# Kernel optimization log

Measured on AMD Instinct MI355X. Metric: run time of the kernel, lower is better.

Reference implementation:

```python
import jax, jax.numpy as jnp
import numpy as np

B, T, S, H, V, MAXL = 8, 128, 256, 1024, 32000, 512
STD = 0.02


def _ln(x, g, b):
    m = jnp.mean(x, -1, keepdims=True)
    v = jnp.mean((x - m) ** 2, -1, keepdims=True)
    return (x - m) / jnp.sqrt(v + 1e-5) * g + b


def setup_inputs() -> dict:
    key = jax.random.key(0)
    ks = jax.random.split(key, 16)
    n = lambda k, shape: jax.random.normal(k, shape, jnp.float32) * STD
    inp = {
        "input_ids": jax.random.randint(ks[0], (B, T), 0, V),
        "encoder_hidden_states": jax.random.normal(ks[1], (B, S, H), jnp.float32),
        "pattern_masks": jax.random.randint(ks[2], (B, T, V), 0, 2).astype(bool),
        "attention_mask": jnp.ones((B, S), bool),
        "tok_emb": n(ks[3], (V, H)),
        "pos_emb": n(ks[4], (MAXL, H)),
        "w_ih": n(ks[5], (4 * H, H)),
        "w_hh": n(ks[6], (4 * H, H)),
        "b_ih": jnp.zeros((4 * H,), jnp.float32),
        "b_hh": jnp.zeros((4 * H,), jnp.float32),
        "wq": n(ks[7], (H, H)), "bq": jnp.zeros((H,), jnp.float32),
        "wk": n(ks[8], (H, H)), "bk": jnp.zeros((H,), jnp.float32),
        "wc": n(ks[9], (H, 2 * H)), "bc": jnp.zeros((H,), jnp.float32),
        "wo": n(ks[10], (V, H)), "bo": jnp.zeros((V,), jnp.float32),
        "g1": n(ks[11], (H,)), "be1": jnp.zeros((H,), jnp.float32),
        "g2": n(ks[12], (H,)), "be2": jnp.zeros((H,), jnp.float32),
    }
    return inp


def reference(input_ids, encoder_hidden_states, pattern_masks, attention_mask,
              tok_emb, pos_emb, w_ih, w_hh, b_ih, b_hh,
              wq, bq, wk, bk, wc, bc, wo, bo, g1, be1, g2, be2):
    # Token + positional embedding (dropout is identity in eval)
    x = tok_emb[input_ids] + pos_emb[:T][None, :, :]  # [B,T,H]

    # Single-layer LSTM (PyTorch gate order i,f,g,o) via scan over time
    def step(carry, xt):
        h, c = carry
        gates = xt @ w_ih.T + b_ih + h @ w_hh.T + b_hh
        i, f, g, o = jnp.split(gates, 4, axis=-1)
        c = jax.nn.sigmoid(f) * c + jax.nn.sigmoid(i) * jnp.tanh(g)
        h = jax.nn.sigmoid(o) * jnp.tanh(c)
        return (h, c), h

    h0 = jnp.zeros((B, H), x.dtype)
    _, hs = jax.lax.scan(step, (h0, h0), jnp.swapaxes(x, 0, 1))
    lstm_out = jnp.swapaxes(hs, 0, 1)  # [B,T,H]

    # Attention: per-position loop in torch == batched over T (keys invariant)
    qn = _ln(lstm_out @ wq.T + bq, g1, be1)              # [B,T,H]
    kn = _ln(encoder_hidden_states @ wk.T + bk, g1, be1)  # [B,S,H]
    scale = H ** (-0.5) * 0.5
    scores = jnp.einsum('bth,bsh->bts', qn, kn) * scale
    am = attention_mask[:, None, :]
    scores = jnp.where(am, scores, -10000.0)
    mx = jnp.max(scores, -1, keepdims=True)
    ex = jnp.exp(scores - mx)
    ex = jnp.where(am, ex, 0.0)
    w = ex / (jnp.sum(ex, -1, keepdims=True) + 1e-6)
    ctx = jnp.einsum('bts,bsh->bth', w, kn)              # [B,T,H]

    hidden = _ln(jnp.concatenate([lstm_out, ctx], -1) @ wc.T + bc, g2, be2)
    logits = hidden @ wo.T + bo                           # [B,T,V]
    logits = jnp.where(pattern_masks, logits, -10000.0)
    return logits
```

## Files before the change

kernel.cpp:

```cpp
#include <hip/hip_runtime.h>
#include <cstdint>
#include <cstddef>

#define Bdim 8
#define Tdim 128
#define Sdim 256
#define Hdim 1024
#define Vdim 32000
#define SENT 0xFFFFFFFFFFFFFFFFULL

typedef unsigned short u16;
typedef unsigned long long u64;
typedef __attribute__((ext_vector_type(8))) short short8;
typedef __attribute__((ext_vector_type(4))) short short4v;
typedef __attribute__((ext_vector_type(4))) float f32x4;
typedef __attribute__((ext_vector_type(2))) unsigned long long u64x2;

union Frag { short8 v; short4v h[2]; };

__device__ __forceinline__ float bf2f(u16 u){
  union { unsigned int i; float f; } x; x.i = ((unsigned int)u) << 16; return x.f;
}
__device__ __forceinline__ u16 f2b(float f){
  union { float f; unsigned int u; } x; x.f = f;
  unsigned int r = x.u + 0x7FFFu + ((x.u >> 16) & 1u);
  return (u16)(r >> 16);
}
__device__ __forceinline__ float ftanh(float x){
  x = fminf(10.f, fmaxf(-10.f, x));
  const float e = __expf(2.f * x);
  return (e - 1.f) / (e + 1.f);
}

__device__ __forceinline__ void gload16(const void* g, void* l){
  __builtin_amdgcn_global_load_lds((const __attribute__((address_space(1))) unsigned int*)g,
                                   (__attribute__((address_space(3))) unsigned int*)l, 16, 0, 0);
}

__device__ __forceinline__ int qsw(int r){ return (r + (r >> 2)) & 3; }

__device__ __forceinline__ u64 aload(const u64* p){
  return __hip_atomic_load(p, __ATOMIC_RELAXED, __HIP_MEMORY_SCOPE_AGENT);
}
__device__ __forceinline__ void astore(u64* p, u64 v){
  __hip_atomic_store(p, v, __ATOMIC_RELAXED, __HIP_MEMORY_SCOPE_AGENT);
}

__global__ __launch_bounds__(256) void detect_bool_k(const unsigned char* __restrict__ p, int* __restrict__ flag){
  __shared__ int s;
  if (threadIdx.x == 0) s = 0;
  __syncthreads();
  int loc = 0;
  for (int i = threadIdx.x; i < 65536; i += 256)
    if ((i & 3) && p[i]) loc = 1;
  if (loc) atomicOr(&s, 1);
  __syncthreads();
  if (threadIdx.x == 0) flag[0] = s;
}

__device__ __forceinline__ bool mask_at(const void* m, size_t idx, int byteflag){
  if (byteflag) return ((const unsigned char*)m)[idx] != 0;
  return ((const int*)m)[idx] != 0;
}

template<typename OutT, bool BF32, int MASK, int NT>
__device__ __forceinline__ void gemm_core(
    char* ldsA0, char* ldsB0, char* ldsA1, char* ldsB1,
    int m0, int n0, int z,
    const u16* __restrict__ A, int lda, long sA,
    const void* __restrict__ Bp, int ldb, long sB,
    OutT* __restrict__ C, int ldc, long sC,
    const float* __restrict__ bias,
    const void* __restrict__ mask,
    const int* __restrict__ mflag,
    int K, float alpha)
{
  const int tid  = threadIdx.x;
  const int lane = tid & 63, wid = tid >> 6;
  const int lm = lane & 15, lg = lane >> 4;
  const int wm = wid >> 1, wn = wid & 1;
  const char* Ab = (const char*)(A + (size_t)z * sA);

  f32x4 acc[4][4 * NT];
#pragma unroll
  for (int i = 0; i < 4; i++)
#pragma unroll
    for (int j = 0; j < 4 * NT; j++) acc[i][j] = (f32x4){0.f, 0.f, 0.f, 0.f};

  const int brow = tid >> 1, bhalf = tid & 1;
  const int qb_st = qsw(brow);

  auto stageA = [&](char* dst, int k0){
    const char* ga = Ab + ((size_t)m0 * lda + k0) * 2;
    const int f0 = tid, f1 = tid + 256;
    const int r0 = f0 >> 2, r1 = f1 >> 2;
    gload16(ga + (size_t)r0 * (lda * 2) + ((f0 & 3) ^ qsw(r0)) * 16, dst + (f0 & ~63) * 16);
    gload16(ga + (size_t)r1 * (lda * 2) + ((f1 & 3) ^ qsw(r1)) * 16, dst + (f1 & ~63) * 16);
  };
  auto stageB16 = [&](char* dst, int k0){
    const char* gbase = (const char*)((const u16*)Bp + (size_t)z * sB);
#pragma unroll
    for (int s = 0; s < NT; s++) {
      const char* gb = gbase + ((size_t)(n0 + s * 128) * ldb + k0) * 2;
      const int f0 = tid, f1 = tid + 256;
      const int r0 = f0 >> 2, r1 = f1 >> 2;
      gload16(gb + (size_t)r0 * (ldb * 2) + ((f0 & 3) ^ qsw(r0)) * 16, dst + s * 8192 + (f0 & ~63) * 16);
      gload16(gb + (size_t)r1 * (ldb * 2) + ((f1 & 3) ^ qsw(r1)) * 16, dst + s * 8192 + (f1 & ~63) * 16);
    }
  };

  float4 nv0, nv1, nv2, nv3;
  auto loadB32 = [&](int k0){
    const float* Bf = (const float*)Bp + (size_t)z * sB;
    const float4* src = (const float4*)(Bf + (size_t)(n0 + brow) * ldb + k0 + bhalf * 16);
    nv0 = src[0]; nv1 = src[1]; nv2 = src[2]; nv3 = src[3];
  };
  auto writeB32 = [&](char* dst){
    union { short8 v; short s[8]; } p0, p1;
    p0.s[0]=(short)f2b(nv0.x); p0.s[1]=(short)f2b(nv0.y); p0.s[2]=(short)f2b(nv0.z); p0.s[3]=(short)f2b(nv0.w);
    p0.s[4]=(short)f2b(nv1.x); p0.s[5]=(short)f2b(nv1.y); p0.s[6]=(short)f2b(nv1.z); p0.s[7]=(short)f2b(nv1.w);
    p1.s[0]=(short)f2b(nv2.x); p1.s[1]=(short)f2b(nv2.y); p1.s[2]=(short)f2b(nv2.z); p1.s[3]=(short)f2b(nv2.w);
    p1.s[4]=(short)f2b(nv3.x); p1.s[5]=(short)f2b(nv3.y); p1.s[6]=(short)f2b(nv3.z); p1.s[7]=(short)f2b(nv3.w);
    char* base = dst + brow * 64;
    *(short8*)(base + (((bhalf * 2 + 0) ^ qb_st) * 16)) = p0.v;
    *(short8*)(base + (((bhalf * 2 + 1) ^ qb_st) * 16)) = p1.v;
  };

  stageA(ldsA0, 0);
  if (BF32) { loadB32(0); writeB32(ldsB0); }
  else stageB16(ldsB0, 0);
  __syncthreads();

  char *cA = ldsA0, *cB = ldsB0, *nA = ldsA1, *nB = ldsB1;
  const int nk = K >> 5;
  for (int i = 0; i < nk; i++) {
    const bool more = (i + 1) < nk;
    if (more) {
      stageA(nA, (i + 1) << 5);
      if (BF32) loadB32((i + 1) << 5);
      else stageB16(nB, (i + 1) << 5);
    }
    Frag a[4];
#pragma unroll
    for (int mi = 0; mi < 4; mi++) {
      const int rr = wm * 64 + mi * 16 + lm;
      const int q = qsw(rr);
      const char* p = cA + rr * 64 + (lg & 1) * 8;
      a[mi].h[0] = *(const short4v*)(p + (((lg >> 1) ^ q) * 16));
      a[mi].h[1] = *(const short4v*)(p + ((((lg >> 1) | 2) ^ q) * 16));
    }
#pragma unroll
    for (int ni = 0; ni < 4 * NT; ni++) {
      const int s = ni >> 2, nl = ni & 3;
      const int rr = wn * 64 + nl * 16 + lm;
      const int q = qsw(rr);
      const char* p = cB + s * 8192 + rr * 64 + (lg & 1) * 8;
      Frag b;
      b.h[0] = *(const short4v*)(p + (((lg >> 1) ^ q) * 16));
      b.h[1] = *(const short4v*)(p + ((((lg >> 1) | 2) ^ q) * 16));
#pragma unroll
      for (int mi = 0; mi < 4; mi++)
        acc[mi][ni] = __builtin_amdgcn_mfma_f32_16x16x32_bf16(a[mi].v, b.v, acc[mi][ni], 0, 0, 0);
    }
    if (BF32 && more) writeB32(nB);
    __syncthreads();
    char* t;
    t = cA; cA = nA; nA = t;
    t = cB; cB = nB; nB = t;
  }

  const int bflag = (MASK == 1) ? *mflag : 0;
#pragma unroll
  for (int mi = 0; mi < 4; mi++) {
#pragma unroll
    for (int ni = 0; ni < 4 * NT; ni++) {
      const int row = m0 + wm * 64 + mi * 16 + lg * 4;
      const int col = n0 + (ni >> 2) * 128 + wn * 64 + (ni & 3) * 16 + lm;
      const float bb = bias ? bias[col] : 0.f;
#pragma unroll
      for (int j = 0; j < 4; j++) {
        float v = acc[mi][ni][j] * alpha + bb;
        const size_t midx = (size_t)(row + j) * ldc + col;
        if (MASK == 1) { if (!mask_at(mask, midx, bflag)) v = -10000.0f; }
        if (MASK == 2) { if (!((const unsigned char*)mask)[midx]) v = -10000.0f; }
        const size_t o = (size_t)z * sC + midx;
        if constexpr (sizeof(OutT) == 2) C[o] = (OutT)f2b(v); else C[o] = (OutT)v;
      }
    }
  }
}

template<typename OutT, bool BF32, int MASK, bool SWAP, int NT = 1>
__global__ __launch_bounds__(256) void gemm_bt(
    const u16* __restrict__ A, int lda, long sA,
    const void* __restrict__ Bp, int ldb, long sB,
    OutT* __restrict__ C, int ldc, long sC,
    const float* __restrict__ bias,
    const void* __restrict__ mask,
    const int* __restrict__ mflag,
    int K, float alpha)
{
  __shared__ alignas(16) char lds[(8192 + 8192 * NT) * 2];
  const int m0 = (SWAP ? blockIdx.x : blockIdx.y) * 128;
  const int n0 = (SWAP ? blockIdx.y : blockIdx.x) * (128 * NT);
  char* ldsA1 = lds + 8192 + 8192 * NT;
  gemm_core<OutT, BF32, MASK, NT>(lds, lds + 8192, ldsA1, ldsA1 + 8192,
      m0, n0, blockIdx.z, A, lda, sA, Bp, ldb, sB, C, ldc, sC,
      bias, mask, mflag, K, alpha);
}

__device__ void lstm_body(char* smem,
    const u16* __restrict__ xpre, const u16* __restrict__ whh,
    u16* __restrict__ hbuf, int bx)
{
  u16* wlds = (u16*)smem;
  u16* hlds = (u16*)(smem + 131072);
  const int tid = threadIdx.x, lane = tid & 63, wid = tid >> 6;
  const int lm = lane & 15, lg = lane >> 4;
  const int gcol0 = bx * 64;

  for (int q = tid; q < 8192; q += 256) {
    const int r = q >> 7, cc = q & 127;
    gload16(whh + (size_t)(gcol0 + r) * 1024 + (size_t)(cc ^ (r & 7)) * 8,
            (char*)wlds + (q & ~63) * 16);
  }

  float c_reg = 0.f;
  const int rloc = wid * 16 + lm, swb = rloc & 7, swa = lm & 7;
  const u16* wl = wlds + rloc * 1024;
  const u16* hl = hlds + swa * 1024;
  const int pk = tid >> 2, qq = tid & 3;
  const u16* xp = xpre + (size_t)(lm * Tdim) * 4096 + gcol0 + wid * 16 + lg * 4;

  for (int t = 0; t < Tdim; t++) {
    u64 xw = 0;
    if (lm < 8) xw = *(const u64*)(xp + (size_t)t * 4096);
    if (t > 0) {
      const u64* ps = (const u64*)(hbuf + ((size_t)(t - 1) * 64 + pk) * 128) + qq * 8;
      u64 w0=SENT,w1=SENT,w2=SENT,w3=SENT,w4=SENT,w5=SENT,w6=SENT,w7=SENT;
      for (;;) {
        if (w0 == SENT) w0 = aload(ps + 0);
        if (w1 == SENT) w1 = aload(ps + 1);
        if (w2 == SENT) w2 = aload(ps + 2);
        if (w3 == SENT) w3 = aload(ps + 3);
        if (w4 == SENT) w4 = aload(ps + 4);
        if (w5 == SENT) w5 = aload(ps + 5);
        if (w6 == SENT) w6 = aload(ps + 6);
        if (w7 == SENT) w7 = aload(ps + 7);
        if (w0 != SENT && w1 != SENT && w2 != SENT && w3 != SENT &&
            w4 != SENT && w5 != SENT && w6 != SENT && w7 != SENT) break;
        __builtin_amdgcn_s_sleep(1);
      }
      {
        const int m = qq * 2;
        u64x2 a; a[0] = w0; a[1] = w1;
        u64x2 b; b[0] = w2; b[1] = w3;
        *(u64x2*)((char*)hlds + m * 2048 + (((pk * 2 + 0) ^ m) * 16)) = a;
        *(u64x2*)((char*)hlds + m * 2048 + (((pk * 2 + 1) ^ m) * 16)) = b;
      }
      {
        const int m = qq * 2 + 1;
        u64x2 a; a[0] = w4; a[1] = w5;
        u64x2 b; b[0] = w6; b[1] = w7;
        *(u64x2*)((char*)hlds + m * 2048 + (((pk * 2 + 0) ^ m) * 16)) = a;
        *(u64x2*)((char*)hlds + m * 2048 + (((pk * 2 + 1) ^ m) * 16)) = b;
      }
    }
    __syncthreads();

    f32x4 acc0, acc1, acc2, acc3;
    {
      union { u64 w; u16 s[4]; } xu; xu.w = xw;
      acc0[0] = bf2f(xu.s[0]); acc0[1] = bf2f(xu.s[1]);
      acc0[2] = bf2f(xu.s[2]); acc0[3] = bf2f(xu.s[3]);
    }
    acc1 = (f32x4){0.f,0.f,0.f,0.f};
    acc2 = (f32x4){0.f,0.f,0.f,0.f};
    acc3 = (f32x4){0.f,0.f,0.f,0.f};

    if (t > 0) {
#pragma unroll
      for (int kk = 0; kk < 32; kk++) {
        const int c0 = kk * 4 + (lg >> 1);
        const int sub = (lg & 1) * 4;
        Frag aw, bh;
        aw.h[0] = *(const short4v*)(wl + ((c0 ^ swb) << 3) + sub);
        aw.h[1] = *(const short4v*)(wl + (((c0 + 2) ^ swb) << 3) + sub);
        bh.h[0] = *(const short4v*)(hl + ((c0 ^ swa) << 3) + sub);
        bh.h[1] = *(const short4v*)(hl + (((c0 + 2) ^ swa) << 3) + sub);
        if ((kk & 3) == 0)      acc0 = __builtin_amdgcn_mfma_f32_16x16x32_bf16(aw.v, bh.v, acc0, 0, 0, 0);
        else if ((kk & 3) == 1) acc1 = __builtin_amdgcn_mfma_f32_16x16x32_bf16(aw.v, bh.v, acc1, 0, 0, 0);
        else if ((kk & 3) == 2) acc2 = __builtin_amdgcn_mfma_f32_16x16x32_bf16(aw.v, bh.v, acc2, 0, 0, 0);
        else                    acc3 = __builtin_amdgcn_mfma_f32_16x16x32_bf16(aw.v, bh.v, acc3, 0, 0, 0);
      }
    }
    const f32x4 g4 = (acc0 + acc1) + (acc2 + acc3);

    const float si = 1.f / (1.f + __expf(-g4[0]));
    const float sf = 1.f / (1.f + __expf(-g4[1]));
    const float so = 1.f / (1.f + __expf(-g4[3]));
    const float cn = sf * c_reg + si * ftanh(g4[2]);
    c_reg = cn;
    const float hn = so * ftanh(cn);
    const int hb = (int)f2b(hn);

    const int v0 = __shfl(hb, lm, 64);
    const int v1 = __shfl(hb, lm + 16, 64);
    const int v2 = __shfl(hb, lm + 32, 64);
    const int v3 = __shfl(hb, lm + 48, 64);
    if (lg == 0 && lm < 8) {
      const u64 pack = (u64)(v0 & 0xFFFF) | ((u64)(v1 & 0xFFFF) << 16)
                     | ((u64)(v2 & 0xFFFF) << 32) | ((u64)(v3 & 0xFFFF) << 48);
      astore((u64*)(hbuf + ((size_t)t * 64 + bx) * 128 + lm * 16 + wid * 4), pack);
    }
    __syncthreads();
  }
}

__global__ __launch_bounds__(256) void lstm_plus(
    const u16* __restrict__ xpre, const u16* __restrict__ whh,
    u16* __restrict__ hbuf,
    const u16* __restrict__ encb, const u16* __restrict__ wkb,
    float* __restrict__ klin, const float* __restrict__ bk,
    const float* __restrict__ wo, u16* __restrict__ wob,
    const void* __restrict__ pmask, unsigned char* __restrict__ pmaskb,
    const int* __restrict__ bflag)
{
  __shared__ alignas(16) char smem[147456];
  const int bx = blockIdx.x;
  if (bx < 64) {
    lstm_body(smem, xpre, whh, hbuf, bx);
  } else if (bx < 192) {
    const int idx = bx - 64;
    gemm_core<float, false, 0, 1>(smem, smem + 8192, smem + 16384, smem + 24576,
        (idx >> 3) * 128, (idx & 7) * 128, 0,
        encb, 1024, 0, wkb, 1024, 0, klin, 1024, 0, bk, nullptr, nullptr, 1024, 1.f);
  } else {
    const int s = bx - 192;
    const int tid = threadIdx.x;
    if (wob) {
      for (int r = s; r < Vdim; r += 64) {
        const size_t i = (size_t)r * 1024 + tid * 4;
        const float4 v = *(const float4*)(wo + i);
        u16* op = wob + i;
        op[0] = f2b(v.x); op[1] = f2b(v.y); op[2] = f2b(v.z); op[3] = f2b(v.w);
      }
    }
    if (pmaskb) {
      const int bfl = *bflag;
      const size_t total = (size_t)Bdim * Tdim * Vdim;
      const size_t nthr = 64 * 256;
      if (bfl == 0) {
        for (size_t i = ((size_t)s * 256 + tid) * 4; i < total; i += nthr * 4) {
          const int4 v = *(const int4*)((const int*)pmask + i);
          uchar4 o;
          o.x = v.x ? 1 : 0; o.y = v.y ? 1 : 0; o.z = v.z ? 1 : 0; o.w = v.w ? 1 : 0;
          *(uchar4*)(pmaskb + i) = o;
        }
      } else {
        for (size_t i = ((size_t)s * 256 + tid) * 16; i < total; i += nthr * 16) {
          *(int4*)(pmaskb + i) = *(const int4*)((const unsigned char*)pmask + i);
        }
      }
    }
  }
}

__global__ __launch_bounds__(256) void hbuf_cat_k(const u16* __restrict__ hbuf, u16* __restrict__ cat){
  const int t = blockIdx.x, tid = threadIdx.x;
  const int p = tid >> 2, q = tid & 3;
  const u64* src = (const u64*)(hbuf + ((size_t)t * 64 + p) * 128);
#pragma unroll
  for (int m = 0; m < 8; m++) {
    const u64 v = src[m * 4 + q];
    *(u64*)(cat + (size_t)(m * Tdim + t) * 2048 + p * 16 + q * 4) = v;
  }
}

__global__ __launch_bounds__(256) void prep_k(
    const float* __restrict__ w_hh, const float* __restrict__ w_ih,
    const float* __restrict__ wq,   const float* __restrict__ wk,
    const float* __restrict__ wc,   const float* __restrict__ enc,
    const int* __restrict__ ids,
    const float* __restrict__ tok,  const float* __restrict__ pos,
    const float* __restrict__ b_ih, const float* __restrict__ b_hh,
    u16* __restrict__ whhb, u16* __restrict__ wihb,
    u16* __restrict__ wqb,  u16* __restrict__ wkb,  u16* __restrict__ wcb,
    u16* __restrict__ encb, u16* __restrict__ xbf,
    float* __restrict__ biasf, u64* __restrict__ hbuf)
{
  const int b = blockIdx.x, tid = threadIdx.x;
  if (b < 8192) {
    const bool ih = b >= 4096;
    const int r = b & 4095;
    const int p = (r & 3) * Hdim + (r >> 2);
    const float4 v = *(const float4*)((ih ? w_ih : w_hh) + (size_t)p * Hdim + tid * 4);
    u16* op = (ih ? wihb : whhb) + (size_t)r * Hdim + tid * 4;
    op[0] = f2b(v.x); op[1] = f2b(v.y); op[2] = f2b(v.z); op[3] = f2b(v.w);
  } else if (b < 9216) {
    const size_t i = (size_t)(b - 8192) * 1024 + tid * 4;
    const float4 v = *(const float4*)(wq + i);
    u16* op = wqb + i;
    op[0] = f2b(v.x); op[1] = f2b(v.y); op[2] = f2b(v.z); op[3] = f2b(v.w);
  } else if (b < 10240) {
    const size_t i = (size_t)(b - 9216) * 1024 + tid * 4;
    const float4 v = *(const float4*)(wk + i);
    u16* op = wkb + i;
    op[0] = f2b(v.x); op[1] = f2b(v.y); op[2] = f2b(v.z); op[3] = f2b(v.w);
  } else if (b < 12288) {
    const size_t i = (size_t)(b - 10240) * 1024 + tid * 4;
    const float4 v = *(const float4*)(wc + i);
    u16* op = wcb + i;
    op[0] = f2b(v.x); op[1] = f2b(v.y); op[2] = f2b(v.z); op[3] = f2b(v.w);
  } else if (b < 14336) {
    const size_t i = (size_t)(b - 12288) * 1024 + tid * 4;
    const float4 v = *(const float4*)(enc + i);
    u16* op = encb + i;
    op[0] = f2b(v.x); op[1] = f2b(v.y); op[2] = f2b(v.z); op[3] = f2b(v.w);
  } else if (b < 15360) {
    const int row = b - 14336;
    const int t = row & (Tdim - 1);
    const int id = ids[row];
    const int h0 = tid * 4;
    const float4 a = *(const float4*)(tok + (size_t)id * Hdim + h0);
    const float4 p = *(const float4*)(pos + (size_t)t * Hdim + h0);
    u16* op = xbf + (size_t)row * Hdim + h0;
    op[0] = f2b(a.x + p.x); op[1] = f2b(a.y + p.y); op[2] = f2b(a.z + p.z); op[3] = f2b(a.w + p.w);
  } else if (b < 15364) {
    const int n0 = (b - 15360) * 1024 + tid * 4;
#pragma unroll
    for (int j = 0; j < 4; j++) {
      const int n = n0 + j;
      const int p = (n & 3) * Hdim + (n >> 2);
      biasf[n] = b_ih[p] + b_hh[p];
    }
  } else {
    const size_t i = ((size_t)(b - 15364) * 256 + tid) * 4;
    u64x2 s2; s2[0] = SENT; s2[1] = SENT;
    *(u64x2*)(hbuf + i)     = s2;
    *(u64x2*)(hbuf + i + 2) = s2;
  }
}

__global__ __launch_bounds__(256) void ln_rows(const float* __restrict__ in, u16* __restrict__ out,
                                               const float* __restrict__ g, const float* __restrict__ be){
  const int row = blockIdx.x, tid = threadIdx.x;
  const int lane = tid & 63, wid = tid >> 6;
  const float4 x = *(const float4*)(in + (size_t)row * Hdim + tid * 4);
  float s = x.x + x.y + x.z + x.w;
  float q = x.x * x.x + x.y * x.y + x.z * x.z + x.w * x.w;
  for (int o = 32; o; o >>= 1) { s += __shfl_down(s, o, 64); q += __shfl_down(q, o, 64); }
  __shared__ float sm[8];
  if (lane == 0) { sm[wid] = s; sm[4 + wid] = q; }
  __syncthreads();
  const float ts = sm[0] + sm[1] + sm[2] + sm[3];
  const float tq = sm[4] + sm[5] + sm[6] + sm[7];
  const float mean = ts * (1.f / Hdim);
  const float var  = tq * (1.f / Hdim) - mean * mean;
  const float r = rsqrtf(var + 1e-5f);
  const int h0 = tid * 4;
  const float4 gv = *(const float4*)(g + h0);
  const float4 bv = *(const float4*)(be + h0);
  u16* op = out + (size_t)row * Hdim + h0;
  op[0] = f2b((x.x - mean) * r * gv.x + bv.x);
  op[1] = f2b((x.y - mean) * r * gv.y + bv.y);
  op[2] = f2b((x.z - mean) * r * gv.z + bv.z);
  op[3] = f2b((x.w - mean) * r * gv.w + bv.w);
}
__global__ __launch_bounds__(256) void softmax_k(const float* __restrict__ sc, const void* __restrict__ am,
                                                 const int* __restrict__ mflag, u16* __restrict__ w){
  const int row = blockIdx.x, tid = threadIdx.x;
  const int lane = tid & 63, wid = tid >> 6;
  const int b = row >> 7;
  const int bflag = *mflag;
  const float v = sc[(size_t)row * Sdim + tid];
  const bool mk = mask_at(am, (size_t)b * Sdim + tid, bflag);
  const float vm = mk ? v : -10000.0f;
  float mx = vm;
  for (int o = 32; o; o >>= 1) mx = fmaxf(mx, __shfl_down(mx, o, 64));
  __shared__ float sm[8];
  if (lane == 0) sm[wid] = mx;
  __syncthreads();
  mx = fmaxf(fmaxf(sm[0], sm[1]), fmaxf(sm[2], sm[3]));
  const float ex = mk ? expf(vm - mx) : 0.f;
  float ss = ex;
  for (int o = 32; o; o >>= 1) ss += __shfl_down(ss, o, 64);
  if (lane == 0) sm[4 + wid] = ss;
  __syncthreads();
  const float tot = sm[4] + sm[5] + sm[6] + sm[7];
  w[(size_t)row * Sdim + tid] = f2b(ex / (tot + 1e-6f));
}
__global__ __launch_bounds__(256) void transp_k(const u16* __restrict__ kn, u16* __restrict__ knT){
  __shared__ u16 tile[64][65];
  const int b = blockIdx.z, h0 = blockIdx.x * 64, s0 = blockIdx.y * 64;
  const u16* src = kn  + (size_t)b * Sdim * Hdim;
  u16* dst       = knT + (size_t)b * Hdim * Sdim;
  for (int e = threadIdx.x; e < 4096; e += 256) {
    const int r = e >> 6, c = e & 63;
    tile[r][c] = src[(size_t)(s0 + r) * Hdim + h0 + c];
  }
  __syncthreads();
  for (int e = threadIdx.x; e < 4096; e += 256) {
    const int hr = e >> 6, scc = e & 63;
    dst[(size_t)(h0 + hr) * Sdim + s0 + scc] = tile[scc][hr];
  }
}

extern "C" void kernel_launch(void* const* d_in, const int* in_sizes, int n_in,
                              void* d_out, int out_size, void* d_ws, size_t ws_size,
                              hipStream_t stream) {
  const int*   input_ids = (const int*)d_in[0];
  const float* enc   = (const float*)d_in[1];
  const void*  pmask = d_in[2];
  const void*  amask = d_in[3];
  const float* tok  = (const float*)d_in[4];
  const float* pos  = (const float*)d_in[5];
  const float* w_ih = (const float*)d_in[6];
  const float* w_hh = (const float*)d_in[7];
  const float* b_ih = (const float*)d_in[8];
  const float* b_hh = (const float*)d_in[9];
  const float* wq = (const float*)d_in[10];
  const float* bq = (const float*)d_in[11];
  const float* wk = (const float*)d_in[12];
  const float* bk = (const float*)d_in[13];
  const float* wc = (const float*)d_in[14];
  const float* bc = (const float*)d_in[15];
  const float* wo = (const float*)d_in[16];
  const float* bo = (const float*)d_in[17];
  const float* g1  = (const float*)d_in[18];
  const float* be1 = (const float*)d_in[19];
  const float* g2  = (const float*)d_in[20];
  const float* be2 = (const float*)d_in[21];
  float* out = (float*)d_out;

  char* ws = (char*)d_ws;
  size_t off = 0;
  auto alloc = [&](size_t b){ size_t o = off; off += (b + 255) & ~(size_t)255; return o; };
  u16*   whhb  = (u16*)  (ws + alloc((size_t)4096 * 1024 * 2));
  u16*   wihb  = (u16*)  (ws + alloc((size_t)4096 * 1024 * 2));
  u16*   wqb   = (u16*)  (ws + alloc((size_t)1024 * 1024 * 2));
  u16*   wkb   = (u16*)  (ws + alloc((size_t)1024 * 1024 * 2));
  u16*   wcb   = (u16*)  (ws + alloc((size_t)1024 * 2048 * 2));
  float* biasf = (float*)(ws + alloc(4096 * 4));
  u16*   xbf   = (u16*)  (ws + alloc((size_t)1024 * 1024 * 2));
  u16*   encb  = (u16*)  (ws + alloc((size_t)2048 * 1024 * 2));
  u16*   xpre  = (u16*)  (ws + alloc((size_t)1024 * 4096 * 2));
  u16*   hbuf  = (u16*)  (ws + alloc((size_t)Tdim * 64 * 128 * 2));
  u16*   cat   = (u16*)  (ws + alloc((size_t)1024 * 2048 * 2));
  float* qlin  = (float*)(ws + alloc((size_t)1024 * 1024 * 4));
  u16*   qn    = (u16*)  (ws + alloc((size_t)1024 * 1024 * 2));
  float* klin  = (float*)(ws + alloc((size_t)2048 * 1024 * 4));
  u16*   kn    = (u16*)  (ws + alloc((size_t)2048 * 1024 * 2));
  u16*   knT   = (u16*)  (ws + alloc((size_t)2048 * 1024 * 2));
  float* scores= (float*)(ws + alloc((size_t)8 * 128 * 256 * 4));
  u16*   attw  = (u16*)  (ws + alloc((size_t)8 * 128 * 256 * 2));
  float* hlin  = (float*)(ws + alloc((size_t)1024 * 1024 * 4));
  u16*   hid   = (u16*)  (ws + alloc((size_t)1024 * 1024 * 2));
  int*   bflag = (int*)  (ws + alloc(256));
  unsigned char* pmaskb = (unsigned char*)(ws + alloc((size_t)Bdim * Tdim * Vdim));
  const bool havePak = off <= ws_size;
  u16*   wob   = (u16*)  (ws + alloc((size_t)Vdim * Hdim * 2));
  const bool haveWob = off <= ws_size;
  if (!havePak) pmaskb = nullptr;
  if (!haveWob) wob = nullptr;
  (void)in_sizes; (void)n_in; (void)out_size;

  detect_bool_k<<<1, 256, 0, stream>>>((const unsigned char*)pmask, bflag);
  prep_k<<<15620, 256, 0, stream>>>(w_hh, w_ih, wq, wk, wc, enc, input_ids,
      tok, pos, b_ih, b_hh, whhb, wihb, wqb, wkb, wcb, encb, xbf, biasf, (u64*)hbuf);

  gemm_bt<u16, false, 0, false><<<dim3(32, 8, 1), 256, 0, stream>>>(
      xbf, 1024, 0, wihb, 1024, 0, xpre, 4096, 0, biasf, nullptr, nullptr, 1024, 1.f);

  lstm_plus<<<256, 256, 0, stream>>>(xpre, whhb, hbuf, encb, wkb, klin, bk,
                                     wo, wob, pmask, pmaskb, bflag);
  hbuf_cat_k<<<Tdim, 256, 0, stream>>>(hbuf, cat);

  gemm_bt<float, false, 0, false><<<dim3(8, 8, 1), 256, 0, stream>>>(
      cat, 2048, 0, wqb, 1024, 0, qlin, 1024, 0, bq, nullptr, nullptr, 1024, 1.f);
  ln_rows<<<1024, 256, 0, stream>>>(qlin, qn, g1, be1);
  ln_rows<<<2048, 256, 0, stream>>>(klin, kn, g1, be1);
  transp_k<<<dim3(16, 4, 8), 256, 0, stream>>>(kn, knT);

  gemm_bt<float, false, 0, false><<<dim3(2, 1, 8), 256, 0, stream>>>(
      qn, 1024, 131072, kn, 1024, 262144, scores, 256, 32768, nullptr, nullptr, nullptr, 1024, 0.015625f);
  softmax_k<<<1024, 256, 0, stream>>>(scores, amask, bflag, attw);
  gemm_bt<u16, false, 0, false><<<dim3(8, 1, 8), 256, 0, stream>>>(
      attw, 256, 32768, knT, 256, 262144, cat + 1024, 2048, 262144, nullptr, nullptr, nullptr, 256, 1.f);

  gemm_bt<float, false, 0, false><<<dim3(8, 8, 1), 256, 0, stream>>>(
      cat, 2048, 0, wcb, 2048, 0, hlin, 1024, 0, bc, nullptr, nullptr, 2048, 1.f);
  ln_rows<<<1024, 256, 0, stream>>>(hlin, hid, g2, be2);

  if (wob && pmaskb)
    gemm_bt<float, false, 2, true, 2><<<dim3(8, 125, 1), 256, 0, stream>>>(
        hid, 1024, 0, wob, 1024, 0, out, 32000, 0, bo, pmaskb, nullptr, 1024, 1.f);
  else if (wob)
    gemm_bt<float, false, 1, true, 2><<<dim3(8, 125, 1), 256, 0, stream>>>(
        hid, 1024, 0, wob, 1024, 0, out, 32000, 0, bo, pmask, bflag, 1024, 1.f);
  else
    gemm_bt<float, true, 1, true><<<dim3(8, 250, 1), 256, 0, stream>>>(
        hid, 1024, 0, wo, 1024, 0, out, 32000, 0, bo, pmask, bflag, 1024, 1.f);
}
```

Before: 842.9 us.

## Fold small kernels into prep and LSTM launches, shrink output GEMM tile

The bool-detection kernel becomes an extra block of prep_k, and the hbuf-to-cat copy kernel is removed because the LSTM blocks now write their hidden states straight into the concat buffer. The wq and wc bf16 conversions move out of prep_k into the idle side blocks of the LSTM launch, where they overlap the recurrent loop. The final vocab GEMM goes from an NT=2 tile to NT=1, doubling its grid. This cuts launch count and serial prep work, at the cost of extra stores inside the latency-bound LSTM loop and less B-tile reuse in the large GEMM.

```diff
diff --git a/kernel.cpp b/kernel.cpp
--- a/kernel.cpp
+++ b/kernel.cpp
@@ -44,18 +44,6 @@
 }
 __device__ __forceinline__ void astore(u64* p, u64 v){
   __hip_atomic_store(p, v, __ATOMIC_RELAXED, __HIP_MEMORY_SCOPE_AGENT);
-}
-
-__global__ __launch_bounds__(256) void detect_bool_k(const unsigned char* __restrict__ p, int* __restrict__ flag){
-  __shared__ int s;
-  if (threadIdx.x == 0) s = 0;
-  __syncthreads();
-  int loc = 0;
-  for (int i = threadIdx.x; i < 65536; i += 256)
-    if ((i & 3) && p[i]) loc = 1;
-  if (loc) atomicOr(&s, 1);
-  __syncthreads();
-  if (threadIdx.x == 0) flag[0] = s;
 }
 
 __device__ __forceinline__ bool mask_at(const void* m, size_t idx, int byteflag){
@@ -211,7 +199,7 @@
 
 __device__ void lstm_body(char* smem,
     const u16* __restrict__ xpre, const u16* __restrict__ whh,
-    u16* __restrict__ hbuf, int bx)
+    u16* __restrict__ hbuf, u16* __restrict__ cat, int bx)
 {
   u16* wlds = (u16*)smem;
   u16* hlds = (u16*)(smem + 131072);
@@ -312,6 +300,7 @@
       const u64 pack = (u64)(v0 & 0xFFFF) | ((u64)(v1 & 0xFFFF) << 16)
                      | ((u64)(v2 & 0xFFFF) << 32) | ((u64)(v3 & 0xFFFF) << 48);
       astore((u64*)(hbuf + ((size_t)t * 64 + bx) * 128 + lm * 16 + wid * 4), pack);
+      *(u64*)(cat + (size_t)(lm * Tdim + t) * 2048 + bx * 16 + wid * 4) = pack;
     }
     __syncthreads();
   }
@@ -319,17 +308,19 @@
 
 __global__ __launch_bounds__(256) void lstm_plus(
     const u16* __restrict__ xpre, const u16* __restrict__ whh,
-    u16* __restrict__ hbuf,
+    u16* __restrict__ hbuf, u16* __restrict__ cat,
     const u16* __restrict__ encb, const u16* __restrict__ wkb,
     float* __restrict__ klin, const float* __restrict__ bk,
     const float* __restrict__ wo, u16* __restrict__ wob,
+    const float* __restrict__ wq, u16* __restrict__ wqb,
+    const float* __restrict__ wc, u16* __restrict__ wcb,
     const void* __restrict__ pmask, unsigned char* __restrict__ pmaskb,
     const int* __restrict__ bflag)
 {
   __shared__ alignas(16) char smem[147456];
   const int bx = blockIdx.x;
   if (bx < 64) {
-    lstm_body(smem, xpre, whh, hbuf, bx);
+    lstm_body(smem, xpre, whh, hbuf, cat, bx);
   } else if (bx < 192) {
     const int idx = bx - 64;
     gemm_core<float, false, 0, 1>(smem, smem + 8192, smem + 16384, smem + 24576,
@@ -338,6 +329,21 @@
   } else {
     const int s = bx - 192;
     const int tid = threadIdx.x;
+    for (int r = s; r < 1024; r += 64) {
+      const size_t i = (size_t)r * 1024 + tid * 4;
+      const float4 v = *(const float4*)(wq + i);
+      u16* op = wqb + i;
+      op[0] = f2b(v.x); op[1] = f2b(v.y); op[2] = f2b(v.z); op[3] = f2b(v.w);
+    }
+    for (int r = s; r < 1024; r += 64) {
+#pragma unroll
+      for (int hc = 0; hc < 2; hc++) {
+        const size_t i = (size_t)r * 2048 + hc * 1024 + tid * 4;
+        const float4 v = *(const float4*)(wc + i);
+        u16* op = wcb + i;
+        op[0] = f2b(v.x); op[1] = f2b(v.y); op[2] = f2b(v.z); op[3] = f2b(v.w);
+      }
+    }
     if (wob) {
       for (int r = s; r < Vdim; r += 64) {
         const size_t i = (size_t)r * 1024 + tid * 4;
@@ -366,29 +372,18 @@
   }
 }
 
-__global__ __launch_bounds__(256) void hbuf_cat_k(const u16* __restrict__ hbuf, u16* __restrict__ cat){
-  const int t = blockIdx.x, tid = threadIdx.x;
-  const int p = tid >> 2, q = tid & 3;
-  const u64* src = (const u64*)(hbuf + ((size_t)t * 64 + p) * 128);
-#pragma unroll
-  for (int m = 0; m < 8; m++) {
-    const u64 v = src[m * 4 + q];
-    *(u64*)(cat + (size_t)(m * Tdim + t) * 2048 + p * 16 + q * 4) = v;
-  }
-}
-
 __global__ __launch_bounds__(256) void prep_k(
     const float* __restrict__ w_hh, const float* __restrict__ w_ih,
-    const float* __restrict__ wq,   const float* __restrict__ wk,
-    const float* __restrict__ wc,   const float* __restrict__ enc,
+    const float* __restrict__ wk,   const float* __restrict__ enc,
     const int* __restrict__ ids,
     const float* __restrict__ tok,  const float* __restrict__ pos,
     const float* __restrict__ b_ih, const float* __restrict__ b_hh,
-    u16* __restrict__ whhb, u16* __restrict__ wihb,
-    u16* __restrict__ wqb,  u16* __restrict__ wkb,  u16* __restrict__ wcb,
+    const unsigned char* __restrict__ pmask,
+    u16* __restrict__ whhb, u16* __restrict__ wihb, u16* __restrict__ wkb,
     u16* __restrict__ encb, u16* __restrict__ xbf,
-    float* __restrict__ biasf, u64* __restrict__ hbuf)
+    float* __restrict__ biasf, u64* __restrict__ hbuf, int* __restrict__ bflag)
 {
+  __shared__ int sdet;
   const int b = blockIdx.x, tid = threadIdx.x;
   if (b < 8192) {
     const bool ih = b >= 4096;
@@ -399,26 +394,16 @@
     op[0] = f2b(v.x); op[1] = f2b(v.y); op[2] = f2b(v.z); op[3] = f2b(v.w);
   } else if (b < 9216) {
     const size_t i = (size_t)(b - 8192) * 1024 + tid * 4;
-    const float4 v = *(const float4*)(wq + i);
-    u16* op = wqb + i;
-    op[0] = f2b(v.x); op[1] = f2b(v.y); op[2] = f2b(v.z); op[3] = f2b(v.w);
-  } else if (b < 10240) {
-    const size_t i = (size_t)(b - 9216) * 1024 + tid * 4;
     const float4 v = *(const float4*)(wk + i);
     u16* op = wkb + i;
     op[0] = f2b(v.x); op[1] = f2b(v.y); op[2] = f2b(v.z); op[3] = f2b(v.w);
-  } else if (b < 12288) {
-    const size_t i = (size_t)(b - 10240) * 1024 + tid * 4;
-    const float4 v = *(const float4*)(wc + i);
-    u16* op = wcb + i;
-    op[0] = f2b(v.x); op[1] = f2b(v.y); op[2] = f2b(v.z); op[3] = f2b(v.w);
-  } else if (b < 14336) {
-    const size_t i = (size_t)(b - 12288) * 1024 + tid * 4;
+  } else if (b < 11264) {
+    const size_t i = (size_t)(b - 9216) * 1024 + tid * 4;
     const float4 v = *(const float4*)(enc + i);
     u16* op = encb + i;
     op[0] = f2b(v.x); op[1] = f2b(v.y); op[2] = f2b(v.z); op[3] = f2b(v.w);
-  } else if (b < 15360) {
-    const int row = b - 14336;
+  } else if (b < 12288) {
+    const int row = b - 11264;
     const int t = row & (Tdim - 1);
     const int id = ids[row];
     const int h0 = tid * 4;
@@ -426,19 +411,28 @@
     const float4 p = *(const float4*)(pos + (size_t)t * Hdim + h0);
     u16* op = xbf + (size_t)row * Hdim + h0;
     op[0] = f2b(a.x + p.x); op[1] = f2b(a.y + p.y); op[2] = f2b(a.z + p.z); op[3] = f2b(a.w + p.w);
-  } else if (b < 15364) {
-    const int n0 = (b - 15360) * 1024 + tid * 4;
+  } else if (b < 12292) {
+    const int n0 = (b - 12288) * 1024 + tid * 4;
 #pragma unroll
     for (int j = 0; j < 4; j++) {
       const int n = n0 + j;
       const int p = (n & 3) * Hdim + (n >> 2);
       biasf[n] = b_ih[p] + b_hh[p];
     }
-  } else {
-    const size_t i = ((size_t)(b - 15364) * 256 + tid) * 4;
+  } else if (b < 12548) {
+    const size_t i = ((size_t)(b - 12292) * 256 + tid) * 4;
     u64x2 s2; s2[0] = SENT; s2[1] = SENT;
     *(u64x2*)(hbuf + i)     = s2;
     *(u64x2*)(hbuf + i + 2) = s2;
+  } else {
+    if (tid == 0) sdet = 0;
+    __syncthreads();
+    int loc = 0;
+    for (int i = tid; i < 65536; i += 256)
+      if ((i & 3) && pmask[i]) loc = 1;
+    if (loc) atomicOr(&sdet, 1);
+    __syncthreads();
+    if (tid == 0) bflag[0] = sdet;
   }
 }
 
@@ -565,16 +559,15 @@
   if (!haveWob) wob = nullptr;
   (void)in_sizes; (void)n_in; (void)out_size;
 
-  detect_bool_k<<<1, 256, 0, stream>>>((const unsigned char*)pmask, bflag);
-  prep_k<<<15620, 256, 0, stream>>>(w_hh, w_ih, wq, wk, wc, enc, input_ids,
-      tok, pos, b_ih, b_hh, whhb, wihb, wqb, wkb, wcb, encb, xbf, biasf, (u64*)hbuf);
+  prep_k<<<12549, 256, 0, stream>>>(w_hh, w_ih, wk, enc, input_ids,
+      tok, pos, b_ih, b_hh, (const unsigned char*)pmask,
+      whhb, wihb, wkb, encb, xbf, biasf, (u64*)hbuf, bflag);
 
   gemm_bt<u16, false, 0, false><<<dim3(32, 8, 1), 256, 0, stream>>>(
       xbf, 1024, 0, wihb, 1024, 0, xpre, 4096, 0, biasf, nullptr, nullptr, 1024, 1.f);
 
-  lstm_plus<<<256, 256, 0, stream>>>(xpre, whhb, hbuf, encb, wkb, klin, bk,
-                                     wo, wob, pmask, pmaskb, bflag);
-  hbuf_cat_k<<<Tdim, 256, 0, stream>>>(hbuf, cat);
+  lstm_plus<<<256, 256, 0, stream>>>(xpre, whhb, hbuf, cat, encb, wkb, klin, bk,
+                                     wo, wob, wq, wqb, wc, wcb, pmask, pmaskb, bflag);
 
   gemm_bt<float, false, 0, false><<<dim3(8, 8, 1), 256, 0, stream>>>(
       cat, 2048, 0, wqb, 1024, 0, qlin, 1024, 0, bq, nullptr, nullptr, 1024, 1.f);
@@ -593,10 +586,10 @@
   ln_rows<<<1024, 256, 0, stream>>>(hlin, hid, g2, be2);
 
   if (wob && pmaskb)
-    gemm_bt<float, false, 2, true, 2><<<dim3(8, 125, 1), 256, 0, stream>>>(
+    gemm_bt<float, false, 2, true><<<dim3(8, 250, 1), 256, 0, stream>>>(
         hid, 1024, 0, wob, 1024, 0, out, 32000, 0, bo, pmaskb, nullptr, 1024, 1.f);
   else if (wob)
-    gemm_bt<float, false, 1, true, 2><<<dim3(8, 125, 1), 256, 0, stream>>>(
+    gemm_bt<float, false, 1, true><<<dim3(8, 250, 1), 256, 0, stream>>>(
         hid, 1024, 0, wob, 1024, 0, out, 32000, 0, bo, pmask, bflag, 1024, 1.f);
   else
     gemm_bt<float, true, 1, true><<<dim3(8, 250, 1), 256, 0, stream>>>(
```

Measured after the change: 800.6 us. 1.05x faster.
